# Kernel optimization log

Measured on AMD Instinct MI355X. Metric: run time of the kernel, lower is better.

Reference implementation:

```python
import jax, jax.numpy as jnp
import numpy as np

MARGIN = 1.0  # from init_kwargs
B, H, W, P = 64, 512, 640, 100000


def setup_inputs() -> dict:
    key = jax.random.key(0)
    k0, k1, k2, k3, k4, k5 = jax.random.split(key, 6)
    return {
        "inp": jax.random.normal(k0, (B, 1, H, W), dtype=jnp.float32),
        "x_A": jax.random.randint(k1, (B, P), 0, W, dtype=jnp.int32),
        "y_A": jax.random.randint(k2, (B, P), 0, H, dtype=jnp.int32),
        "x_B": jax.random.randint(k3, (B, P), 0, W, dtype=jnp.int32),
        "y_B": jax.random.randint(k4, (B, P), 0, H, dtype=jnp.int32),
        "ordinal": jax.random.randint(k5, (B, P), 0, 3, dtype=jnp.int32),
    }


def reference(inp, x_A, y_A, x_B, y_B, ordinal):
    # inp: [B,1,H,W]; point coords: [B,P]; ordinal in {0,1,2} -> gt in {-1,0,1}
    depth = inp[:, 0]                                   # [B,H,W]
    bidx = jnp.arange(depth.shape[0])[:, None]          # [B,1]
    z_A = depth[bidx, y_A, x_A]                         # [B,P] gather
    z_B = depth[bidx, y_B, x_B]                         # [B,P] gather
    gt = (ordinal - 1).astype(depth.dtype)              # {-1,0,1}
    mask = jnp.abs(gt)
    zd = z_A - z_B
    m = jnp.asarray(MARGIN, depth.dtype)
    # ordered pairs: log(1+exp(-min(gt*zd, m))); equal pairs: max(zd^2, m^2)
    loss = mask * jnp.log(1.0 + jnp.exp(-jnp.minimum(gt * zd, m))) \
         + (1.0 - mask) * jnp.maximum(zd * zd, m * m)
    n_point_total = depth.shape[0] * x_A.shape[1]
    return jnp.sum(loss) / n_point_total
```

## Files before the change

### kernel.cpp

```cpp
#include <hip/hip_runtime.h>


constexpr int B = 64;
constexpr int H = 512;
constexpr int W = 640;
constexpr int P = 100000;
constexpr int SEGS = 4;
constexpr int SEGP = P / SEGS;
constexpr int NT = 512;
constexpr int K = (SEGP + NT - 1) / NT;
constexpr int TAIL_T = SEGP - (K - 1) * NT;
constexpr int SROWS = 48;
constexpr int NS = (H + SROWS - 1) / SROWS;
constexpr int SELEMS = SROWS * W;
constexpr int LELEMS = (H - (NS - 1) * SROWS) * W;
constexpr int PF = SELEMS / (NT * 4);
constexpr int PF_LAST = LELEMS / (NT * 4);
constexpr int NBLK = B * SEGS;
constexpr float INV_N = 1.0f / (float)(B * P);

typedef float vfloat4 __attribute__((ext_vector_type(4)));

__device__ __forceinline__ unsigned bf16_rnd(float f) {
    return (__builtin_bit_cast(unsigned, f) + 0x8000u) >> 16;
}

__global__ __launch_bounds__(NT, 1) void rdc_kernel(
        const float* __restrict__ depth,
        const int* __restrict__ xA, const int* __restrict__ yA,
        const int* __restrict__ xB, const int* __restrict__ yB,
        const int* __restrict__ ord,
        float* __restrict__ partials) {
    __shared__ unsigned short stripe[SELEMS];
    __shared__ float wsum[8];

    int j = blockIdx.x;
    int x = j & 7;
    int g = j >> 3;
    int b = (g >> 2) * 8 + x;
    int c = g & 3;
    int t = threadIdx.x;

    const float* slab = depth + (size_t)b * (H * W);
    int base_pt = b * P + c * SEGP;

    int offA[K], offB[K];
    unsigned zAB[K];
    unsigned rankW[2] = {0u, 0u};
    unsigned signW[2] = {0u, 0u};
    #pragma unroll
    for (int k = 0; k < K; ++k) {
        int pl = k * NT + t;
        if (k == K - 1 && pl >= SEGP) pl = SEGP - 1;
        int gi = base_pt + pl;
        int xa = __builtin_nontemporal_load(&xA[gi]);
        int ya = __builtin_nontemporal_load(&yA[gi]);
        int xb = __builtin_nontemporal_load(&xB[gi]);
        int yb = __builtin_nontemporal_load(&yB[gi]);
        int od = __builtin_nontemporal_load(&ord[gi]);
        offA[k] = ya * W + xa;
        offB[k] = yb * W + xb;
        rankW[k >> 5] |= (unsigned)(od != 1) << (k & 31);
        signW[k >> 5] |= (unsigned)(od == 2) << (k & 31);
        zAB[k] = 0u;
    }

    vfloat4 pf[PF];
    #pragma unroll
    for (int i = 0; i < PF; ++i)
        pf[i] = *(const vfloat4*)(slab + ((i * NT + t) << 2));
    #pragma unroll
    for (int i = 0; i < PF; ++i) {
        uint2 pk;
        pk.x = bf16_rnd(pf[i].x) | (bf16_rnd(pf[i].y) << 16);
        pk.y = bf16_rnd(pf[i].z) | (bf16_rnd(pf[i].w) << 16);
        *(uint2*)&stripe[(i * NT + t) << 2] = pk;
    }
    __syncthreads();

    for (int s = 0; s < NS; ++s) {
        int npf = 0;
        if (s + 1 < NS) {
            int gbase = (s + 1) * SELEMS;
            npf = (s + 1 == NS - 1) ? PF_LAST : PF;
            #pragma unroll
            for (int i = 0; i < PF; ++i)
                if (i < npf)
                    pf[i] = *(const vfloat4*)(slab + gbase + ((i * NT + t) << 2));
        }

        unsigned base = (unsigned)(s * SELEMS);
        unsigned span = (s == NS - 1) ? (unsigned)LELEMS : (unsigned)SELEMS;
        #pragma unroll
        for (int k = 0; k < K; ++k) {
            unsigned la = (unsigned)offA[k] - base;
            unsigned va = (unsigned)stripe[la < span ? la : 0u];
            zAB[k] = (la < span) ? ((zAB[k] & 0xFFFF0000u) | va) : zAB[k];
            unsigned lb = (unsigned)offB[k] - base;
            unsigned vb = (unsigned)stripe[lb < span ? lb : 0u];
            zAB[k] = (lb < span) ? ((zAB[k] & 0x0000FFFFu) | (vb << 16)) : zAB[k];
        }
        __syncthreads();

        if (s + 1 < NS) {
            #pragma unroll
            for (int i = 0; i < PF; ++i)
                if (i < npf) {
                    uint2 pk;
                    pk.x = bf16_rnd(pf[i].x) | (bf16_rnd(pf[i].y) << 16);
                    pk.y = bf16_rnd(pf[i].z) | (bf16_rnd(pf[i].w) << 16);
                    *(uint2*)&stripe[(i * NT + t) << 2] = pk;
                }
            __syncthreads();
        }
    }

    float tailf = (t < TAIL_T) ? 1.0f : 0.0f;
    float acc = 0.0f;
    #pragma unroll
    for (int k = 0; k < K; ++k) {
        float za = __builtin_bit_cast(float, zAB[k] << 16);
        float zb = __builtin_bit_cast(float, zAB[k] & 0xFFFF0000u);
        float zd = za - zb;
        unsigned rb = (rankW[k >> 5] >> (k & 31)) & 1u;
        unsigned sb = (signW[k >> 5] >> (k & 31)) & 1u;
        float gzd = sb ? zd : -zd;
        float lr = __logf(1.0f + __expf(-fminf(gzd, 1.0f)));
        float le = fmaxf(zd * zd, 1.0f);
        float l = rb ? lr : le;
        if (k == K - 1) l *= tailf;
        acc += l;
    }

    #pragma unroll
    for (int o = 32; o > 0; o >>= 1)
        acc += __shfl_down(acc, o, 64);
    int lane = t & 63;
    int wid  = t >> 6;
    if (lane == 0) wsum[wid] = acc;
    __syncthreads();
    if (wid == 0 && lane == 0) {
        float v = 0.0f;
        #pragma unroll
        for (int w = 0; w < 8; ++w) v += wsum[w];
        partials[j] = v;
    }
}

__global__ __launch_bounds__(256) void rdc_finalize(
        const float* __restrict__ partials, float* __restrict__ out, int n) {
    float acc = 0.0f;
    for (int k = threadIdx.x; k < n; k += 256)
        acc += partials[k];
    #pragma unroll
    for (int o = 32; o > 0; o >>= 1)
        acc += __shfl_down(acc, o, 64);
    __shared__ float wsum[4];
    int lane = threadIdx.x & 63;
    int wid  = threadIdx.x >> 6;
    if (lane == 0) wsum[wid] = acc;
    __syncthreads();
    if (wid == 0 && lane == 0)
        out[0] = (wsum[0] + wsum[1] + wsum[2] + wsum[3]) * INV_N;
}

extern "C" void kernel_launch(void* const* d_in, const int* in_sizes, int n_in,
                              void* d_out, int out_size, void* d_ws, size_t ws_size,
                              hipStream_t stream) {
    const float* depth = (const float*)d_in[0];
    const int* xA = (const int*)d_in[1];
    const int* yA = (const int*)d_in[2];
    const int* xB = (const int*)d_in[3];
    const int* yB = (const int*)d_in[4];
    const int* ord = (const int*)d_in[5];
    float* out = (float*)d_out;

    float* partials = (float*)d_ws;
    rdc_kernel<<<NBLK, NT, 0, stream>>>(depth, xA, yA, xB, yB, ord, partials);
    rdc_finalize<<<1, 256, 0, stream>>>(partials, out, NBLK);
}
```

Before: 298.9 us.

## Split each batch into eight point segments with vectorized index loads

Doubles the number of point segments per batch, giving 512 blocks instead of 256. Each block still streams the full depth slab into LDS as bf16, but holds half as many points per thread. Point index and ordinal arrays are now read as 4-wide int vectors, and the launch attributes target two waves per EU so two blocks can share a CU. The cost is that each depth slab is read from global memory twice as many times in total, which adds memory traffic in exchange for more parallelism and lower register pressure.

```diff
diff --git a/kernel.cpp b/kernel.cpp
--- a/kernel.cpp
+++ b/kernel.cpp
@@ -5,11 +5,13 @@
 constexpr int H = 512;
 constexpr int W = 640;
 constexpr int P = 100000;
-constexpr int SEGS = 4;
+constexpr int SEGS = 8;
 constexpr int SEGP = P / SEGS;
 constexpr int NT = 512;
-constexpr int K = (SEGP + NT - 1) / NT;
-constexpr int TAIL_T = SEGP - (K - 1) * NT;
+constexpr int G4 = SEGP / 4;
+constexpr int KG = (G4 + NT - 1) / NT;
+constexpr int TAIL_T = G4 - (KG - 1) * NT;
+constexpr int KS = KG * 4;
 constexpr int SROWS = 48;
 constexpr int NS = (H + SROWS - 1) / SROWS;
 constexpr int SELEMS = SROWS * W;
@@ -20,16 +22,19 @@
 constexpr float INV_N = 1.0f / (float)(B * P);
 
 typedef float vfloat4 __attribute__((ext_vector_type(4)));
+typedef int vint4 __attribute__((ext_vector_type(4)));
 
 __device__ __forceinline__ unsigned bf16_rnd(float f) {
     return (__builtin_bit_cast(unsigned, f) + 0x8000u) >> 16;
 }
 
-__global__ __launch_bounds__(NT, 1) void rdc_kernel(
+__global__ __attribute__((amdgpu_flat_work_group_size(NT, NT),
+                          amdgpu_waves_per_eu(2, 2)))
+void rdc_kernel(
         const float* __restrict__ depth,
-        const int* __restrict__ xA, const int* __restrict__ yA,
-        const int* __restrict__ xB, const int* __restrict__ yB,
-        const int* __restrict__ ord,
+        const vint4* __restrict__ xA4, const vint4* __restrict__ yA4,
+        const vint4* __restrict__ xB4, const vint4* __restrict__ yB4,
+        const vint4* __restrict__ ord4,
         float* __restrict__ partials) {
     __shared__ unsigned short stripe[SELEMS];
     __shared__ float wsum[8];
@@ -37,32 +42,41 @@
     int j = blockIdx.x;
     int x = j & 7;
     int g = j >> 3;
-    int b = (g >> 2) * 8 + x;
-    int c = g & 3;
+    int b = ((g >> 3) << 3) | x;
+    int c = g & 7;
     int t = threadIdx.x;
 
     const float* slab = depth + (size_t)b * (H * W);
-    int base_pt = b * P + c * SEGP;
+    int base_i4 = (b * P + c * SEGP) >> 2;
 
-    int offA[K], offB[K];
-    unsigned zAB[K];
-    unsigned rankW[2] = {0u, 0u};
-    unsigned signW[2] = {0u, 0u};
+    int offA[KS], offB[KS];
+    unsigned zAB[KS];
+    unsigned rankW = 0u;
+    unsigned signW = 0u;
     #pragma unroll
-    for (int k = 0; k < K; ++k) {
-        int pl = k * NT + t;
-        if (k == K - 1 && pl >= SEGP) pl = SEGP - 1;
-        int gi = base_pt + pl;
-        int xa = __builtin_nontemporal_load(&xA[gi]);
-        int ya = __builtin_nontemporal_load(&yA[gi]);
-        int xb = __builtin_nontemporal_load(&xB[gi]);
-        int yb = __builtin_nontemporal_load(&yB[gi]);
-        int od = __builtin_nontemporal_load(&ord[gi]);
-        offA[k] = ya * W + xa;
-        offB[k] = yb * W + xb;
-        rankW[k >> 5] |= (unsigned)(od != 1) << (k & 31);
-        signW[k >> 5] |= (unsigned)(od == 2) << (k & 31);
-        zAB[k] = 0u;
+    for (int k = 0; k < KG; ++k) {
+        int gl = k * NT + t;
+        if (k == KG - 1 && gl >= G4) gl = G4 - 1;
+        int gi = base_i4 + gl;
+        vint4 xa = __builtin_nontemporal_load(&xA4[gi]);
+        vint4 ya = __builtin_nontemporal_load(&yA4[gi]);
+        vint4 xb = __builtin_nontemporal_load(&xB4[gi]);
+        vint4 yb = __builtin_nontemporal_load(&yB4[gi]);
+        vint4 od = __builtin_nontemporal_load(&ord4[gi]);
+        int s0 = 4 * k;
+        offA[s0+0] = ya.x * W + xa.x;  offB[s0+0] = yb.x * W + xb.x;
+        offA[s0+1] = ya.y * W + xa.y;  offB[s0+1] = yb.y * W + xb.y;
+        offA[s0+2] = ya.z * W + xa.z;  offB[s0+2] = yb.z * W + xb.z;
+        offA[s0+3] = ya.w * W + xa.w;  offB[s0+3] = yb.w * W + xb.w;
+        rankW |= (unsigned)(od.x != 1) << (s0+0);
+        rankW |= (unsigned)(od.y != 1) << (s0+1);
+        rankW |= (unsigned)(od.z != 1) << (s0+2);
+        rankW |= (unsigned)(od.w != 1) << (s0+3);
+        signW |= (unsigned)(od.x == 2) << (s0+0);
+        signW |= (unsigned)(od.y == 2) << (s0+1);
+        signW |= (unsigned)(od.z == 2) << (s0+2);
+        signW |= (unsigned)(od.w == 2) << (s0+3);
+        zAB[s0+0] = 0u; zAB[s0+1] = 0u; zAB[s0+2] = 0u; zAB[s0+3] = 0u;
     }
 
     vfloat4 pf[PF];
@@ -79,20 +93,17 @@
     __syncthreads();
 
     for (int s = 0; s < NS; ++s) {
-        int npf = 0;
-        if (s + 1 < NS) {
-            int gbase = (s + 1) * SELEMS;
-            npf = (s + 1 == NS - 1) ? PF_LAST : PF;
-            #pragma unroll
-            for (int i = 0; i < PF; ++i)
-                if (i < npf)
-                    pf[i] = *(const vfloat4*)(slab + gbase + ((i * NT + t) << 2));
-        }
+        int npf = (s + 1 < NS) ? ((s + 1 == NS - 1) ? PF_LAST : PF) : 0;
+        int gbase = (s + 1) * SELEMS;
+        #pragma unroll
+        for (int i = 0; i < PF; ++i)
+            if (i < npf)
+                pf[i] = *(const vfloat4*)(slab + gbase + ((i * NT + t) << 2));
 
         unsigned base = (unsigned)(s * SELEMS);
         unsigned span = (s == NS - 1) ? (unsigned)LELEMS : (unsigned)SELEMS;
         #pragma unroll
-        for (int k = 0; k < K; ++k) {
+        for (int k = 0; k < KS; ++k) {
             unsigned la = (unsigned)offA[k] - base;
             unsigned va = (unsigned)stripe[la < span ? la : 0u];
             zAB[k] = (la < span) ? ((zAB[k] & 0xFFFF0000u) | va) : zAB[k];
@@ -102,7 +113,7 @@
         }
         __syncthreads();
 
-        if (s + 1 < NS) {
+        if (npf) {
             #pragma unroll
             for (int i = 0; i < PF; ++i)
                 if (i < npf) {
@@ -115,21 +126,23 @@
         }
     }
 
-    float tailf = (t < TAIL_T) ? 1.0f : 0.0f;
     float acc = 0.0f;
     #pragma unroll
-    for (int k = 0; k < K; ++k) {
-        float za = __builtin_bit_cast(float, zAB[k] << 16);
-        float zb = __builtin_bit_cast(float, zAB[k] & 0xFFFF0000u);
-        float zd = za - zb;
-        unsigned rb = (rankW[k >> 5] >> (k & 31)) & 1u;
-        unsigned sb = (signW[k >> 5] >> (k & 31)) & 1u;
-        float gzd = sb ? zd : -zd;
-        float lr = __logf(1.0f + __expf(-fminf(gzd, 1.0f)));
-        float le = fmaxf(zd * zd, 1.0f);
-        float l = rb ? lr : le;
-        if (k == K - 1) l *= tailf;
-        acc += l;
+    for (int k = 0; k < KG; ++k) {
+        float gmask = (k < KG - 1 || t < TAIL_T) ? 1.0f : 0.0f;
+        #pragma unroll
+        for (int m = 0; m < 4; ++m) {
+            int s = 4 * k + m;
+            float za = __builtin_bit_cast(float, zAB[s] << 16);
+            float zb = __builtin_bit_cast(float, zAB[s] & 0xFFFF0000u);
+            float zd = za - zb;
+            unsigned rb = (rankW >> s) & 1u;
+            unsigned sb = (signW >> s) & 1u;
+            float gzd = sb ? zd : -zd;
+            float lr = __logf(1.0f + __expf(-fminf(gzd, 1.0f)));
+            float le = fmaxf(zd * zd, 1.0f);
+            acc += gmask * (rb ? lr : le);
+        }
     }
 
     #pragma unroll
@@ -168,14 +181,14 @@
                               void* d_out, int out_size, void* d_ws, size_t ws_size,
                               hipStream_t stream) {
     const float* depth = (const float*)d_in[0];
-    const int* xA = (const int*)d_in[1];
-    const int* yA = (const int*)d_in[2];
-    const int* xB = (const int*)d_in[3];
-    const int* yB = (const int*)d_in[4];
-    const int* ord = (const int*)d_in[5];
+    const vint4* xA4 = (const vint4*)d_in[1];
+    const vint4* yA4 = (const vint4*)d_in[2];
+    const vint4* xB4 = (const vint4*)d_in[3];
+    const vint4* yB4 = (const vint4*)d_in[4];
+    const vint4* ord4 = (const vint4*)d_in[5];
     float* out = (float*)d_out;
 
     float* partials = (float*)d_ws;
-    rdc_kernel<<<NBLK, NT, 0, stream>>>(depth, xA, yA, xB, yB, ord, partials);
+    rdc_kernel<<<NBLK, NT, 0, stream>>>(depth, xA4, yA4, xB4, yB4, ord4, partials);
     rdc_finalize<<<1, 256, 0, stream>>>(partials, out, NBLK);
 }
```

After: 293.5 us. No clear change (-1.8%).
